# Kernel tuning notes

Hardware: AMD Instinct MI355X
Metric: run time of the kernel (lower is better)

## Reference

```python
import jax, jax.numpy as jnp
import numpy as np

NUM_HEADS = 16
GRID_SIZE = 16


def rotate(x, pos):
    # x: [B, nH, N, D] with D even; pos: [N] float
    D = x.shape[-1]
    half = D // 2
    omega = jnp.arange(half, dtype=x.dtype) / half
    omega = 1.0 / (10000.0 ** omega)
    freq = pos[:, None].astype(x.dtype) * omega          # [N, half]
    # torch .repeat(1,1,1,2) TILES the last dim (not interleave)
    emb_sin = jnp.tile(jnp.sin(freq), (1, 2))            # [N, D]
    emb_cos = jnp.tile(jnp.cos(freq), (1, 2))
    y = x.reshape(x.shape[:-1] + (half, 2))
    rot = jnp.stack((-y[..., 1], y[..., 0]), axis=-1).reshape(x.shape)
    return x * emb_cos + rot * emb_sin


def setup_inputs() -> dict:
    key = jax.random.key(0)
    k1, k2, k3, k4 = jax.random.split(key, 4)
    B, N, C = 2, 2048, 1024
    return {
        "x": jax.random.normal(k1, (B, N, C), dtype=jnp.float32),
        "W_qkv": jax.random.normal(k2, (3 * C, C), dtype=jnp.float32) * 0.02,
        "W_proj": jax.random.normal(k3, (C, C), dtype=jnp.float32) * 0.02,
        "b_proj": jax.random.normal(k4, (C,), dtype=jnp.float32) * 0.02,
        "T": 8,
        "H": 16,
        "W": 16,
    }


def reference(x, W_qkv, W_proj, b_proj, T, H, W):
    B, N, C = x.shape
    nH = NUM_HEADS
    hd = C // nH
    d_dim = 2 * (hd // 3 // 2)   # 20 for hd=64
    h_dim = d_dim
    w_dim = d_dim

    # axial positions (mask=None path): ids = arange(T*H*W)
    ids = jnp.arange(T * H * W)
    d_pos = (ids // (H * W)).astype(jnp.float32)
    rem = ids % (H * W)
    h_pos = (rem // W).astype(jnp.float32) * (GRID_SIZE / H)
    w_pos = (rem % W).astype(jnp.float32) * (GRID_SIZE / W)

    # fused QKV projection (no bias)
    qkv = jnp.einsum('bnc,oc->bno', x, W_qkv)            # [B, N, 3C]
    qkv = qkv.reshape(B, N, 3, nH, hd).transpose(2, 0, 3, 1, 4)
    q, k, v = qkv[0], qkv[1], qkv[2]                     # [B, nH, N, hd]

    s0, s1, s2 = 0, d_dim, d_dim + h_dim
    s3 = s2 + w_dim
    qd = rotate(q[..., s0:s1], d_pos); kd = rotate(k[..., s0:s1], d_pos)
    qh = rotate(q[..., s1:s2], h_pos); kh = rotate(k[..., s1:s2], h_pos)
    qw = rotate(q[..., s2:s3], w_pos); kw = rotate(k[..., s2:s3], w_pos)
    if s3 < hd:
        q = jnp.concatenate([qd, qh, qw, q[..., s3:]], axis=-1)
        k = jnp.concatenate([kd, kh, kw, k[..., s3:]], axis=-1)
    else:
        q = jnp.concatenate([qd, qh, qw], axis=-1)
        k = jnp.concatenate([kd, kh, kw], axis=-1)

    # SDPA (default scale = hd**-0.5, no dropout, not causal)
    scale = hd ** (-0.5)
    scores = jnp.einsum('bhqd,bhkd->bhqk', q, k) * scale
    attn = jax.nn.softmax(scores, axis=-1)
    out = jnp.einsum('bhqk,bhkd->bhqd', attn, v)          # [B, nH, N, hd]

    out = out.transpose(0, 2, 1, 3).reshape(B, N, C)
    out = jnp.einsum('bnc,oc->bno', out, W_proj) + b_proj
    return out


if __name__ == "__main__":
    inp = setup_inputs()
    y = reference(**inp)
    print(y.shape, y.dtype)
```

## Files before the change

kernel.cpp:

```cpp
#include <hip/hip_runtime.h>
#include <stdint.h>

typedef unsigned short u16;
typedef __attribute__((ext_vector_type(8))) short bf16x8;
typedef __attribute__((ext_vector_type(4))) float f32x4;

#define DEVI static __device__ __forceinline__

static constexpr int NTOK = 2048;
static constexpr int CDIM = 1024;
static constexpr int C3   = 3072;

DEVI u16 f2bf(float f) {
  uint32_t u = __float_as_uint(f);
  return (u16)((u + 0x7fffu + ((u >> 16) & 1u)) >> 16);
}

DEVI float exp2fast(float x) { return __builtin_amdgcn_exp2f(x); }

DEVI void gl_lds16(const void* g, void* l) {
  __builtin_amdgcn_global_load_lds(
      (__attribute__((address_space(1))) uint32_t*)g,
      (__attribute__((address_space(3))) uint32_t*)l, 16, 0, 0);
}

DEVI f32x4 mfma16(bf16x8 a, bf16x8 b, f32x4 c) {
  return __builtin_amdgcn_mfma_f32_16x16x32_bf16(a, b, c, 0, 0, 0);
}

__global__ void k_cvt3(const float* __restrict__ x, const float* __restrict__ wq,
                       const float* __restrict__ wp, u16* __restrict__ xb,
                       u16* __restrict__ wqb, u16* __restrict__ wpb) {
  int i = (blockIdx.x * blockDim.x + threadIdx.x) * 4;
  const float* src; u16* dst; int off;
  if (i < 4194304)      { src = x;  dst = xb;  off = i; }
  else if (i < 7340032) { src = wq; dst = wqb; off = i - 4194304; }
  else                  { src = wp; dst = wpb; off = i - 7340032; }
  float4 v = *reinterpret_cast<const float4*>(src + off);
  ushort4 o;
  o.x = f2bf(v.x); o.y = f2bf(v.y); o.z = f2bf(v.z); o.w = f2bf(v.w);
  *reinterpret_cast<ushort4*>(dst + off) = o;
}

template<int MODE>
__global__ __launch_bounds__(256, 2) void k_gemm(
    const u16* __restrict__ A, const u16* __restrict__ Bw,
    float* __restrict__ Cout, const float* __restrict__ bias,
    u16* __restrict__ qb, u16* __restrict__ kb, u16* __restrict__ vT,
    int Nn, int K) {
  __shared__ u16 smem[MODE == 2 ? 17408 : 8192];
  u16* Al = smem;
  u16* Bl = smem + 4096;
  const int tid = threadIdx.x, wid = tid >> 6, lane = tid & 63;
  const int bm = blockIdx.x, bn = blockIdx.y;
  const int wr = wid >> 1, wc = wid & 1;
  const int fr = lane & 15, fg = lane >> 4;
  f32x4 acc[4][4] = {};

  const int r0 = wid * 16 + (lane >> 2);
  const int c0 = (lane & 3) * 8;
  const u16* Ag = A + (size_t)(bm * 128) * K + c0;
  const u16* Bg = Bw + (size_t)(bn * 128) * K + c0;
  u16* Alb = Al + wid * 512;
  u16* Blb = Bl + wid * 512;
  const int fk = fg * 8;

  for (int kt = 0; kt < K; kt += 32) {
    __syncthreads();
    gl_lds16(Ag + (size_t)r0 * K + kt,        Alb);
    gl_lds16(Ag + (size_t)(64 + r0) * K + kt, Alb + 2048);
    gl_lds16(Bg + (size_t)r0 * K + kt,        Blb);
    gl_lds16(Bg + (size_t)(64 + r0) * K + kt, Blb + 2048);
    __syncthreads();
    bf16x8 af[4], bfr[4];
#pragma unroll
    for (int i = 0; i < 4; ++i)
      af[i] = *reinterpret_cast<const bf16x8*>(&Al[(wr * 64 + i * 16 + fr) * 32 + fk]);
#pragma unroll
    for (int j = 0; j < 4; ++j)
      bfr[j] = *reinterpret_cast<const bf16x8*>(&Bl[(wc * 64 + j * 16 + fr) * 32 + fk]);
#pragma unroll
    for (int i = 0; i < 4; ++i)
#pragma unroll
      for (int j = 0; j < 4; ++j)
        acc[i][j] = mfma16(af[i], bfr[j], acc[i][j]);
  }
  const int orow0 = bm * 128 + wr * 64 + fg * 4;

  if constexpr (MODE == 1) {
    const int ocol0 = bn * 128 + wc * 64 + fr;
#pragma unroll
    for (int j = 0; j < 4; ++j) {
      int col = ocol0 + j * 16;
      float badd = bias[col];
#pragma unroll
      for (int i = 0; i < 4; ++i)
#pragma unroll
        for (int r = 0; r < 4; ++r)
          Cout[(size_t)(orow0 + i * 16 + r) * Nn + col] = acc[i][j][r] + badd;
    }
  } else {
    const int which = bn >> 3;
    if (which < 2) {
      const int cbase = (bn & 7) * 128 + wc * 64 + fr;
      u16* dst = (which == 0) ? qb : kb;
#pragma unroll
      for (int j = 0; j < 4; ++j) {
        const int c = cbase + j * 16;
        const int d = c & 63, hh = c >> 6;
        const bool dorope = (d < 60);
        int seg = 0; float omega = 0.f;
        if (dorope) {
          seg = d / 20;
          int ds = d - seg * 20;
          int jj = (ds >= 10) ? ds - 10 : ds;
          omega = exp2fast(-1.3287712379549449f * (float)jj);
        }
#pragma unroll
        for (int i = 0; i < 4; ++i) {
#pragma unroll
          for (int r = 0; r < 4; ++r) {
            const int m = orow0 + i * 16 + r;
            const int b = m >> 11, n = m & (NTOK - 1);
            float val = acc[i][j][r];
            float pr = __shfl_xor(val, 1, 64);
            float outv = val;
            if (dorope) {
              float pos = (seg == 0) ? (float)(n >> 8)
                        : (seg == 1) ? (float)((n >> 4) & 15)
                                     : (float)(n & 15);
              float f = pos * omega, sn, cs;
              __sincosf(f, &sn, &cs);
              outv = (d & 1) ? val * cs + pr * sn : val * cs - pr * sn;
            }
            if (which == 0) outv *= 0.18033688011112042f;
            dst[((size_t)(b * 16 + hh) * NTOK + n) * 64 + d] = f2bf(outv);
          }
        }
      }
    } else {
      __syncthreads();
      const int mbase = wr * 64 + fg * 4;
#pragma unroll
      for (int j = 0; j < 4; ++j) {
        const int crow = wc * 64 + j * 16 + fr;
#pragma unroll
        for (int i = 0; i < 4; ++i) {
          ushort4 pk;
          pk.x = f2bf(acc[i][j][0]); pk.y = f2bf(acc[i][j][1]);
          pk.z = f2bf(acc[i][j][2]); pk.w = f2bf(acc[i][j][3]);
          *reinterpret_cast<ushort4*>(&smem[crow * 136 + mbase + i * 16]) = pk;
        }
      }
      __syncthreads();
      const int c = tid >> 1, mh = (tid & 1) * 64;
      const int cfull = (bn & 7) * 128 + c;
      const int hh = cfull >> 6, d = cfull & 63;
      const int b = bm >> 4;
      u16* dst = vT + (((size_t)(b * 16 + hh)) * 64 + d) * NTOK + (bm & 15) * 128 + mh;
      const u16* srcl = &smem[c * 136 + mh];
#pragma unroll
      for (int s = 0; s < 8; ++s)
        *reinterpret_cast<bf16x8*>(dst + s * 8) = *reinterpret_cast<const bf16x8*>(srcl + s * 8);
    }
  }
}

__global__ __launch_bounds__(256, 2) void k_attn(
    const u16* __restrict__ qb, const u16* __restrict__ kb,
    const u16* __restrict__ vT, u16* __restrict__ outb) {
  __shared__ u16 Kl[2][64 * 64];
  __shared__ u16 Vl[2][64 * 64];
  __shared__ u16 Pl[4][32 * 64];
  const int bh = blockIdx.x;
  const int qt = blockIdx.y;
  const int tid = threadIdx.x, wid = tid >> 6, lane = tid & 63;
  const int fr = lane & 15, fg = lane >> 4;
  const int swz = fr & 7;

  bf16x8 qf[2][2];
  const u16* qbase = qb + ((size_t)bh * NTOK + qt * 128 + wid * 32 + fr) * 64;
#pragma unroll
  for (int qa = 0; qa < 2; ++qa)
#pragma unroll
    for (int h = 0; h < 2; ++h)
      qf[qa][h] = *reinterpret_cast<const bf16x8*>(qbase + qa * 1024 + h * 32 + fg * 8);

  f32x4 acc[2][4] = {};
  float mrun[2] = {-1e30f, -1e30f}, lrun[2] = {0.f, 0.f};

  const int srow = lane >> 3;
  const int scol = ((lane & 7) ^ srow) * 8;
  const u16* kg = kb + ((size_t)bh * NTOK + wid * 8 + srow) * 64 + scol;
  const u16* vg = vT + ((size_t)bh * 64 + wid * 8 + srow) * NTOK + scol;
  u16* Pw = &Pl[wid][0];

  auto stage = [&](int buf, int kvt) {
#pragma unroll
    for (int s = 0; s < 2; ++s) {
      gl_lds16(kg + (size_t)(kvt + s * 32) * 64, &Kl[buf][s * 2048 + wid * 512]);
      gl_lds16(vg + (size_t)(s * 32) * NTOK + kvt, &Vl[buf][s * 2048 + wid * 512]);
    }
  };

  stage(0, 0);
  __syncthreads();
  int cur = 0;
  for (int kvt = 0; kvt < NTOK; kvt += 64) {
    if (kvt + 64 < NTOK) stage(cur ^ 1, kvt + 64);
    const u16* Kc = &Kl[cur][0];
    const u16* Vc = &Vl[cur][0];

    bf16x8 kf[4][2], vf[4][2];
#pragma unroll
    for (int mf = 0; mf < 4; ++mf) {
      int rb = (mf * 16 + fr) * 64;
#pragma unroll
      for (int h = 0; h < 2; ++h)
        kf[mf][h] = *reinterpret_cast<const bf16x8*>(Kc + rb + (((h * 4 + fg) ^ swz) * 8));
    }
#pragma unroll
    for (int nf = 0; nf < 4; ++nf) {
      int rb = (nf * 16 + fr) * 64;
#pragma unroll
      for (int ks = 0; ks < 2; ++ks)
        vf[nf][ks] = *reinterpret_cast<const bf16x8*>(Vc + rb + (((ks * 4 + fg) ^ swz) * 8));
    }

    f32x4 st[2][4];
    __builtin_amdgcn_s_setprio(1);
#pragma unroll
    for (int qa = 0; qa < 2; ++qa)
#pragma unroll
      for (int mf = 0; mf < 4; ++mf) {
        f32x4 s0 = {};
        s0 = mfma16(kf[mf][0], qf[qa][0], s0);
        s0 = mfma16(kf[mf][1], qf[qa][1], s0);
        st[qa][mf] = s0;
      }
    __builtin_amdgcn_s_setprio(0);

#pragma unroll
    for (int qa = 0; qa < 2; ++qa) {
      float t0 = fmaxf(fmaxf(st[qa][0][0], st[qa][0][1]), fmaxf(st[qa][0][2], st[qa][0][3]));
      float t1 = fmaxf(fmaxf(st[qa][1][0], st[qa][1][1]), fmaxf(st[qa][1][2], st[qa][1][3]));
      float t2 = fmaxf(fmaxf(st[qa][2][0], st[qa][2][1]), fmaxf(st[qa][2][2], st[qa][2][3]));
      float t3 = fmaxf(fmaxf(st[qa][3][0], st[qa][3][1]), fmaxf(st[qa][3][2], st[qa][3][3]));
      float tm = fmaxf(fmaxf(t0, t1), fmaxf(t2, t3));
      tm = fmaxf(tm, __shfl_xor(tm, 16, 64));
      tm = fmaxf(tm, __shfl_xor(tm, 32, 64));
      bool skip = (__all(tm - mrun[qa] <= 8.f) != 0);
      float corr, mref;
      if (skip) {
        corr = 1.f; mref = mrun[qa];
      } else {
        float mnew = fmaxf(mrun[qa], tm);
        corr = exp2fast(mrun[qa] - mnew);
        mrun[qa] = mnew; mref = mnew;
      }
      float ps = 0.f;
      const int prow = qa * 16 + fr;
#pragma unroll
      for (int mf = 0; mf < 4; ++mf) {
        float p0 = exp2fast(st[qa][mf][0] - mref);
        float p1 = exp2fast(st[qa][mf][1] - mref);
        float p2 = exp2fast(st[qa][mf][2] - mref);
        float p3 = exp2fast(st[qa][mf][3] - mref);
        ps += (p0 + p1) + (p2 + p3);
        uint32_t k0, k1;
        asm("v_cvt_pk_bf16_f32 %0, %1, %2" : "=v"(k0) : "v"(p0), "v"(p1));
        asm("v_cvt_pk_bf16_f32 %0, %1, %2" : "=v"(k1) : "v"(p2), "v"(p3));
        int c16 = (mf * 2 + (fg >> 1)) ^ swz;
        uint2 val; val.x = k0; val.y = k1;
        *reinterpret_cast<uint2*>(Pw + prow * 64 + c16 * 8 + (fg & 1) * 4) = val;
      }
      ps += __shfl_xor(ps, 16, 64);
      ps += __shfl_xor(ps, 32, 64);
      lrun[qa] = lrun[qa] * corr + ps;

      asm volatile("" ::: "memory");

      if (!skip) {
        float cr[4];
#pragma unroll
        for (int r = 0; r < 4; ++r) cr[r] = __shfl(corr, fg * 4 + r, 64);
#pragma unroll
        for (int nf = 0; nf < 4; ++nf)
#pragma unroll
          for (int r = 0; r < 4; ++r) acc[qa][nf][r] *= cr[r];
      }
      bf16x8 pa[2];
#pragma unroll
      for (int ks = 0; ks < 2; ++ks)
        pa[ks] = *reinterpret_cast<const bf16x8*>(Pw + prow * 64 + (((ks * 4 + fg) ^ swz) * 8));
      __builtin_amdgcn_s_setprio(1);
#pragma unroll
      for (int nf = 0; nf < 4; ++nf)
#pragma unroll
        for (int ks = 0; ks < 2; ++ks)
          acc[qa][nf] = mfma16(pa[ks], vf[nf][ks], acc[qa][nf]);
      __builtin_amdgcn_s_setprio(0);
    }
    __syncthreads();
    cur ^= 1;
  }

  const int b = bh >> 4, h = bh & 15;
#pragma unroll
  for (int qa = 0; qa < 2; ++qa) {
    float linv[4];
#pragma unroll
    for (int r = 0; r < 4; ++r) linv[r] = 1.f / __shfl(lrun[qa], fg * 4 + r, 64);
#pragma unroll
    for (int nf = 0; nf < 4; ++nf)
#pragma unroll
      for (int r = 0; r < 4; ++r) {
        int n = qt * 128 + wid * 32 + qa * 16 + fg * 4 + r;
        int col = h * 64 + nf * 16 + fr;
        outb[((size_t)b * NTOK + n) * CDIM + col] = f2bf(acc[qa][nf][r] * linv[r]);
      }
  }
}

extern "C" void kernel_launch(void* const* d_in, const int* in_sizes, int n_in,
                              void* d_out, int out_size, void* d_ws, size_t ws_size,
                              hipStream_t stream) {
  (void)in_sizes; (void)n_in; (void)out_size; (void)ws_size;
  const float* x  = (const float*)d_in[0];
  const float* Wq = (const float*)d_in[1];
  const float* Wp = (const float*)d_in[2];
  const float* bp = (const float*)d_in[3];

  char* w = (char*)d_ws;
  u16* x_bf  = (u16*)(w + 0);
  u16* wq_bf = (u16*)(w + 8388608);
  u16* wp_bf = (u16*)(w + 14680064);
  u16* q_bf  = (u16*)(w + 16777216);
  u16* k_bf  = (u16*)(w + 25165824);
  u16* vT    = (u16*)(w + 33554432);
  u16* at_bf = (u16*)(w + 41943040);

  k_cvt3<<<8192, 256, 0, stream>>>(x, Wq, Wp, x_bf, wq_bf, wp_bf);

  k_gemm<2><<<dim3(32, 24), 256, 0, stream>>>(x_bf, wq_bf, nullptr, nullptr,
                                              q_bf, k_bf, vT, C3, CDIM);

  k_attn<<<dim3(32, 16), 256, 0, stream>>>(q_bf, k_bf, vT, at_bf);

  k_gemm<1><<<dim3(32, 8), 256, 0, stream>>>(at_bf, wp_bf, (float*)d_out, bp,
                                             nullptr, nullptr, nullptr, CDIM, CDIM);
}
```

Baseline: 128.3 us.

## Halve attention query tile per block to double grid and occupancy

The attention kernel now has each wave handle 16 query rows instead of 32, so a block covers 64 queries and the grid doubles to 32x32 blocks. Launch bounds rise to 4 blocks per CU and the P scratch buffer shrinks. The goal is more resident waves to hide latency and fill all CUs. The cost is that every K/V tile is staged into shared memory twice as often per query, and each MFMA on the loaded K/V fragments is reused half as much.

```diff
diff --git a/kernel.cpp b/kernel.cpp
--- a/kernel.cpp
+++ b/kernel.cpp
@@ -166,28 +166,26 @@
   }
 }
 
-__global__ __launch_bounds__(256, 2) void k_attn(
+__global__ __launch_bounds__(256, 4) void k_attn(
     const u16* __restrict__ qb, const u16* __restrict__ kb,
     const u16* __restrict__ vT, u16* __restrict__ outb) {
   __shared__ u16 Kl[2][64 * 64];
   __shared__ u16 Vl[2][64 * 64];
-  __shared__ u16 Pl[4][32 * 64];
+  __shared__ u16 Pl[4][16 * 64];
   const int bh = blockIdx.x;
   const int qt = blockIdx.y;
   const int tid = threadIdx.x, wid = tid >> 6, lane = tid & 63;
   const int fr = lane & 15, fg = lane >> 4;
   const int swz = fr & 7;
 
-  bf16x8 qf[2][2];
-  const u16* qbase = qb + ((size_t)bh * NTOK + qt * 128 + wid * 32 + fr) * 64;
-#pragma unroll
-  for (int qa = 0; qa < 2; ++qa)
-#pragma unroll
-    for (int h = 0; h < 2; ++h)
-      qf[qa][h] = *reinterpret_cast<const bf16x8*>(qbase + qa * 1024 + h * 32 + fg * 8);
-
-  f32x4 acc[2][4] = {};
-  float mrun[2] = {-1e30f, -1e30f}, lrun[2] = {0.f, 0.f};
+  bf16x8 qf[2];
+  const u16* qbase = qb + ((size_t)bh * NTOK + qt * 64 + wid * 16 + fr) * 64;
+#pragma unroll
+  for (int h = 0; h < 2; ++h)
+    qf[h] = *reinterpret_cast<const bf16x8*>(qbase + h * 32 + fg * 8);
+
+  f32x4 acc[4] = {};
+  float mrun = -1e30f, lrun = 0.f;
 
   const int srow = lane >> 3;
   const int scol = ((lane & 7) ^ srow) * 8;
@@ -227,99 +225,91 @@
         vf[nf][ks] = *reinterpret_cast<const bf16x8*>(Vc + rb + (((ks * 4 + fg) ^ swz) * 8));
     }
 
-    f32x4 st[2][4];
+    f32x4 st[4];
     __builtin_amdgcn_s_setprio(1);
 #pragma unroll
-    for (int qa = 0; qa < 2; ++qa)
-#pragma unroll
-      for (int mf = 0; mf < 4; ++mf) {
-        f32x4 s0 = {};
-        s0 = mfma16(kf[mf][0], qf[qa][0], s0);
-        s0 = mfma16(kf[mf][1], qf[qa][1], s0);
-        st[qa][mf] = s0;
-      }
+    for (int mf = 0; mf < 4; ++mf) {
+      f32x4 s0 = {};
+      s0 = mfma16(kf[mf][0], qf[0], s0);
+      s0 = mfma16(kf[mf][1], qf[1], s0);
+      st[mf] = s0;
+    }
     __builtin_amdgcn_s_setprio(0);
 
-#pragma unroll
-    for (int qa = 0; qa < 2; ++qa) {
-      float t0 = fmaxf(fmaxf(st[qa][0][0], st[qa][0][1]), fmaxf(st[qa][0][2], st[qa][0][3]));
-      float t1 = fmaxf(fmaxf(st[qa][1][0], st[qa][1][1]), fmaxf(st[qa][1][2], st[qa][1][3]));
-      float t2 = fmaxf(fmaxf(st[qa][2][0], st[qa][2][1]), fmaxf(st[qa][2][2], st[qa][2][3]));
-      float t3 = fmaxf(fmaxf(st[qa][3][0], st[qa][3][1]), fmaxf(st[qa][3][2], st[qa][3][3]));
-      float tm = fmaxf(fmaxf(t0, t1), fmaxf(t2, t3));
-      tm = fmaxf(tm, __shfl_xor(tm, 16, 64));
-      tm = fmaxf(tm, __shfl_xor(tm, 32, 64));
-      bool skip = (__all(tm - mrun[qa] <= 8.f) != 0);
-      float corr, mref;
-      if (skip) {
-        corr = 1.f; mref = mrun[qa];
-      } else {
-        float mnew = fmaxf(mrun[qa], tm);
-        corr = exp2fast(mrun[qa] - mnew);
-        mrun[qa] = mnew; mref = mnew;
-      }
-      float ps = 0.f;
-      const int prow = qa * 16 + fr;
-#pragma unroll
-      for (int mf = 0; mf < 4; ++mf) {
-        float p0 = exp2fast(st[qa][mf][0] - mref);
-        float p1 = exp2fast(st[qa][mf][1] - mref);
-        float p2 = exp2fast(st[qa][mf][2] - mref);
-        float p3 = exp2fast(st[qa][mf][3] - mref);
-        ps += (p0 + p1) + (p2 + p3);
-        uint32_t k0, k1;
-        asm("v_cvt_pk_bf16_f32 %0, %1, %2" : "=v"(k0) : "v"(p0), "v"(p1));
-        asm("v_cvt_pk_bf16_f32 %0, %1, %2" : "=v"(k1) : "v"(p2), "v"(p3));
-        int c16 = (mf * 2 + (fg >> 1)) ^ swz;
-        uint2 val; val.x = k0; val.y = k1;
-        *reinterpret_cast<uint2*>(Pw + prow * 64 + c16 * 8 + (fg & 1) * 4) = val;
-      }
-      ps += __shfl_xor(ps, 16, 64);
-      ps += __shfl_xor(ps, 32, 64);
-      lrun[qa] = lrun[qa] * corr + ps;
-
-      asm volatile("" ::: "memory");
-
-      if (!skip) {
-        float cr[4];
-#pragma unroll
-        for (int r = 0; r < 4; ++r) cr[r] = __shfl(corr, fg * 4 + r, 64);
-#pragma unroll
-        for (int nf = 0; nf < 4; ++nf)
-#pragma unroll
-          for (int r = 0; r < 4; ++r) acc[qa][nf][r] *= cr[r];
-      }
-      bf16x8 pa[2];
+    float t0 = fmaxf(fmaxf(st[0][0], st[0][1]), fmaxf(st[0][2], st[0][3]));
+    float t1 = fmaxf(fmaxf(st[1][0], st[1][1]), fmaxf(st[1][2], st[1][3]));
+    float t2 = fmaxf(fmaxf(st[2][0], st[2][1]), fmaxf(st[2][2], st[2][3]));
+    float t3 = fmaxf(fmaxf(st[3][0], st[3][1]), fmaxf(st[3][2], st[3][3]));
+    float tm = fmaxf(fmaxf(t0, t1), fmaxf(t2, t3));
+    tm = fmaxf(tm, __shfl_xor(tm, 16, 64));
+    tm = fmaxf(tm, __shfl_xor(tm, 32, 64));
+    bool skip = (__all(tm - mrun <= 8.f) != 0);
+    float corr, mref;
+    if (skip) {
+      corr = 1.f; mref = mrun;
+    } else {
+      float mnew = fmaxf(mrun, tm);
+      corr = exp2fast(mrun - mnew);
+      mrun = mnew; mref = mnew;
+    }
+    float ps = 0.f;
+#pragma unroll
+    for (int mf = 0; mf < 4; ++mf) {
+      float p0 = exp2fast(st[mf][0] - mref);
+      float p1 = exp2fast(st[mf][1] - mref);
+      float p2 = exp2fast(st[mf][2] - mref);
+      float p3 = exp2fast(st[mf][3] - mref);
+      ps += (p0 + p1) + (p2 + p3);
+      uint32_t k0, k1;
+      asm("v_cvt_pk_bf16_f32 %0, %1, %2" : "=v"(k0) : "v"(p0), "v"(p1));
+      asm("v_cvt_pk_bf16_f32 %0, %1, %2" : "=v"(k1) : "v"(p2), "v"(p3));
+      int c16 = (mf * 2 + (fg >> 1)) ^ swz;
+      uint2 val; val.x = k0; val.y = k1;
+      *reinterpret_cast<uint2*>(Pw + fr * 64 + c16 * 8 + (fg & 1) * 4) = val;
+    }
+    ps += __shfl_xor(ps, 16, 64);
+    ps += __shfl_xor(ps, 32, 64);
+    lrun = lrun * corr + ps;
+
+    asm volatile("" ::: "memory");
+
+    if (!skip) {
+      float cr[4];
+#pragma unroll
+      for (int r = 0; r < 4; ++r) cr[r] = __shfl(corr, fg * 4 + r, 64);
+#pragma unroll
+      for (int nf = 0; nf < 4; ++nf)
+#pragma unroll
+        for (int r = 0; r < 4; ++r) acc[nf][r] *= cr[r];
+    }
+    bf16x8 pa[2];
+#pragma unroll
+    for (int ks = 0; ks < 2; ++ks)
+      pa[ks] = *reinterpret_cast<const bf16x8*>(Pw + fr * 64 + (((ks * 4 + fg) ^ swz) * 8));
+    __builtin_amdgcn_s_setprio(1);
+#pragma unroll
+    for (int nf = 0; nf < 4; ++nf)
 #pragma unroll
       for (int ks = 0; ks < 2; ++ks)
-        pa[ks] = *reinterpret_cast<const bf16x8*>(Pw + prow * 64 + (((ks * 4 + fg) ^ swz) * 8));
-      __builtin_amdgcn_s_setprio(1);
-#pragma unroll
-      for (int nf = 0; nf < 4; ++nf)
-#pragma unroll
-        for (int ks = 0; ks < 2; ++ks)
-          acc[qa][nf] = mfma16(pa[ks], vf[nf][ks], acc[qa][nf]);
-      __builtin_amdgcn_s_setprio(0);
-    }
+        acc[nf] = mfma16(pa[ks], vf[nf][ks], acc[nf]);
+    __builtin_amdgcn_s_setprio(0);
+
     __syncthreads();
     cur ^= 1;
   }
 
   const int b = bh >> 4, h = bh & 15;
-#pragma unroll
-  for (int qa = 0; qa < 2; ++qa) {
-    float linv[4];
-#pragma unroll
-    for (int r = 0; r < 4; ++r) linv[r] = 1.f / __shfl(lrun[qa], fg * 4 + r, 64);
-#pragma unroll
-    for (int nf = 0; nf < 4; ++nf)
-#pragma unroll
-      for (int r = 0; r < 4; ++r) {
-        int n = qt * 128 + wid * 32 + qa * 16 + fg * 4 + r;
-        int col = h * 64 + nf * 16 + fr;
-        outb[((size_t)b * NTOK + n) * CDIM + col] = f2bf(acc[qa][nf][r] * linv[r]);
-      }
-  }
+  float linv[4];
+#pragma unroll
+  for (int r = 0; r < 4; ++r) linv[r] = 1.f / __shfl(lrun, fg * 4 + r, 64);
+#pragma unroll
+  for (int nf = 0; nf < 4; ++nf)
+#pragma unroll
+    for (int r = 0; r < 4; ++r) {
+      int n = qt * 64 + wid * 16 + fg * 4 + r;
+      int col = h * 64 + nf * 16 + fr;
+      outb[((size_t)b * NTOK + n) * CDIM + col] = f2bf(acc[nf][r] * linv[r]);
+    }
 }
 
 extern "C" void kernel_launch(void* const* d_in, const int* in_sizes, int n_in,
@@ -345,7 +335,7 @@
   k_gemm<2><<<dim3(32, 24), 256, 0, stream>>>(x_bf, wq_bf, nullptr, nullptr,
                                               q_bf, k_bf, vT, C3, CDIM);
 
-  k_attn<<<dim3(32, 16), 256, 0, stream>>>(q_bf, k_bf, vT, at_bf);
+  k_attn<<<dim3(32, 32), 256, 0, stream>>>(q_bf, k_bf, vT, at_bf);
 
   k_gemm<1><<<dim3(32, 8), 256, 0, stream>>>(at_bf, wp_bf, (float*)d_out, bp,
                                              nullptr, nullptr, nullptr, CDIM, CDIM);
```

Measured after the change: 134.7 us. +5.0%, slower.
